# Optimization experiments

Hardware: AMD Instinct MI355X
Metric: run time of the kernel (lower is better)

The kernel has to match this reference:

```python
import jax, jax.numpy as jnp
import numpy as np

REGIONS = [(0, 16), (17, 21), (22, 26), (27, 30), (31, 35), (36, 41), (42, 47), (48, 59), (60, 67)]
LN_EPS = 1e-5


def setup_inputs() -> dict:
    key = jax.random.key(0)
    ks = jax.random.split(key, 8)
    B, T, N, D = 32, 128, 68, 128
    sc = 1.0 / np.sqrt(D)
    inp = {
        "lm_data": jax.random.normal(ks[0], (B, T, N, D), jnp.float32),
        "adj": jax.random.uniform(ks[1], (77, 77), jnp.float32) / 77.0,
        "Wr": jax.random.normal(ks[2], (D, 1), jnp.float32) * sc,
        "br": jnp.zeros((1,), jnp.float32),
        "W0": jax.random.normal(ks[3], (D, D), jnp.float32) * sc,
        "b0": jnp.zeros((D,), jnp.float32),
        "W1": jax.random.normal(ks[4], (D, D), jnp.float32) * sc,
        "b1": jnp.zeros((D,), jnp.float32),
        "W2": jax.random.normal(ks[5], (D, D), jnp.float32) * sc,
        "b2": jnp.zeros((D,), jnp.float32),
        "W3": jax.random.normal(ks[6], (D, D), jnp.float32) * sc,
        "b3": jnp.zeros((D,), jnp.float32),
        "gamma": jnp.ones((D,), jnp.float32),
        "beta": jnp.zeros((D,), jnp.float32),
    }
    return inp


def _region_pool(x, Wr, br):
    # x: [B,T,R,D] -> attention-pooled [B,T,D]
    scores = jnp.einsum('btrd,do->btro', x, Wr) + br  # [B,T,R,1]
    w = jax.nn.softmax(scores, axis=-2)
    return jnp.sum(w * x, axis=-2)


def reference(lm_data, adj, Wr, br, W0, b0, W1, b1, W2, b2, W3, b3, gamma, beta):
    # init_global_nodes: gather each region, attention-pool, scatter into 9 global nodes
    global_nodes = jnp.stack(
        [_region_pool(lm_data[..., s:e + 1, :], Wr, br) for s, e in REGIONS], axis=2
    )  # [B,T,9,D]
    x = jnp.concatenate([lm_data, global_nodes], axis=2)  # [B,T,77,D]

    # 4-layer residual GCN: relu(Linear(adj @ x))
    layers = [(W0, b0), (W1, b1), (W2, b2), (W3, b3)]
    residual = x
    for i, (W, b) in enumerate(layers):
        agg = jnp.einsum('nm,btmd->btnd', adj, x)
        out = jax.nn.relu(agg @ W + b)
        if i < len(layers) - 1:
            out = out + residual  # feature dims all equal
            residual = out
        x = out

    # LayerNorm (dropout is identity at eval)
    mu = jnp.mean(x, axis=-1, keepdims=True)
    var = jnp.var(x, axis=-1, keepdims=True)
    x = (x - mu) / jnp.sqrt(var + LN_EPS) * gamma + beta
    return x
```

## Files before the change

### kernel.cpp

```cpp
#include <hip/hip_runtime.h>
#include <stdint.h>

typedef __attribute__((ext_vector_type(8))) short bf16x8;
typedef __attribute__((ext_vector_type(4))) float f32x4;
typedef unsigned short u16;
typedef __attribute__((ext_vector_type(4))) unsigned short us4;
typedef __attribute__((ext_vector_type(8))) unsigned short us8;

#define NP 80

__device__ __constant__ int c_RS[9] = {0, 17, 22, 27, 31, 36, 42, 48, 60};
__device__ __constant__ int c_RE[9] = {16, 21, 26, 30, 35, 41, 47, 59, 67};

__device__ __forceinline__ float b2f(u16 h) {
    union { unsigned int u; float f; } v;
    v.u = ((unsigned int)h) << 16;
    return v.f;
}
__device__ __forceinline__ u16 f2b(float f) {
    union { float f; unsigned int u; } v;
    v.f = f;
    unsigned int r = v.u + 0x7fffu + ((v.u >> 16) & 1u);
    return (u16)(r >> 16);
}
__device__ __forceinline__ int agx(int row, int col) {
    return row * 128 + (col ^ (((row & 4) << 3) | ((row & 8) << 1)));
}

__global__ void prep_kernel(const float* __restrict__ adj,
                            const float* __restrict__ W0, const float* __restrict__ W1,
                            const float* __restrict__ W2, const float* __restrict__ W3,
                            u16* __restrict__ adjp, u16* __restrict__ WT) {
    int id = blockIdx.x * 256 + threadIdx.x;
    if (id < 80 * 96) {
        int m = id / 96, c = id - m * 96;
        float v = 0.f;
        if (m < 77) {
            int k = (c < 64) ? c : (c - 16);
            if (c >= 64 && c < 80) k = 77;
            if (k < 77) v = adj[m * 77 + k];
        }
        adjp[id] = f2b(v);
    }
    {
        int l = id >> 14, r = id & 16383;
        int n = r >> 7, k = r & 127;
        const float* W = (l == 0) ? W0 : (l == 1) ? W1 : (l == 2) ? W2 : W3;
        WT[id] = f2b(W[k * 128 + n]);
    }
}

__global__ __launch_bounds__(256, 4) void gcn_kernel(
    const float* __restrict__ lm, const float* __restrict__ Wr,
    const float* __restrict__ b0, const float* __restrict__ b1,
    const float* __restrict__ b2, const float* __restrict__ b3,
    const float* __restrict__ gamma, const float* __restrict__ beta,
    const u16* __restrict__ adjp, const u16* __restrict__ WT,
    float* __restrict__ out) {
    __shared__ __align__(16) u16 xT[128 * NP];
    __shared__ __align__(16) u16 ag[80 * 128];

    const int t = threadIdx.x;
    const int lane = t & 63;
    const int w = t >> 6;
    const int lo = lane & 15;
    const int qd = lane >> 4;
    const size_t pos = blockIdx.x;
    const float* lmp = lm + pos * (68 * 128);

    float* WrF = (float*)&ag[68 * 128];
    float* scoreS = (float*)&ag[70 * 128];
    float* muP = (float*)xT;
    float* rsP = muP + 80;

    if (t < 128) {
        WrF[t] = Wr[t];
        xT[t * NP + 77] = 0; xT[t * NP + 78] = 0; xT[t * NP + 79] = 0;
    }
    const float4* lmp4 = (const float4*)lmp;
    for (int c = t; c < 68 * 32; c += 256) {
        int n = c >> 5, q = c & 31;
        float4 v = lmp4[c];
        us4 o;
        o[0] = f2b(v.x); o[1] = f2b(v.y); o[2] = f2b(v.z); o[3] = f2b(v.w);
        *(us4*)(&ag[agx(n, q * 4)]) = o;
    }
    __syncthreads();

    for (int c = t; c < 68 * 16; c += 256) {
        int d8 = c / 68, n = c - d8 * 68;
        us8 v = *(const us8*)(&ag[agx(n, d8 * 8)]);
#pragma unroll
        for (int j = 0; j < 8; j++) xT[(d8 * 8 + j) * NP + n] = v[j];
    }
    if (t < 68) {
        float s = 0.f;
        for (int d8 = 0; d8 < 16; d8++) {
            us8 v = *(const us8*)(&ag[agx(t, d8 * 8)]);
#pragma unroll
            for (int j = 0; j < 8; j++) s += b2f(v[j]) * WrF[d8 * 8 + j];
        }
        scoreS[t] = s;
    }
    __syncthreads();

    for (int c = t; c < 9 * 128; c += 256) {
        int r = c >> 7, d = c & 127;
        int s0 = c_RS[r], e0 = c_RE[r];
        float mx = -3e38f;
        for (int i = s0; i <= e0; i++) mx = fmaxf(mx, scoreS[i]);
        float sum = 0.f, g = 0.f;
        for (int i = s0; i <= e0; i++) {
            float e = __expf(scoreS[i] - mx);
            sum += e;
            g += e * b2f(ag[agx(i, d)]);
        }
        xT[d * NP + 68 + r] = f2b(g / sum);
    }
    __syncthreads();

    for (int l = 0; l < 4; l++) {
        f32x4 acc[5][2];
#pragma unroll
        for (int a = 0; a < 5; a++)
#pragma unroll
            for (int j = 0; j < 2; j++)
#pragma unroll
                for (int r = 0; r < 4; r++) acc[a][j][r] = 0.f;
#pragma unroll
        for (int ks = 0; ks < 3; ks++) {
            const int koff = (ks == 2) ? 48 : ks * 32;
            bf16x8 bA[5], bB[2];
#pragma unroll
            for (int tm = 0; tm < 5; tm++)
                bA[tm] = *(const bf16x8*)(adjp + (tm * 16 + lo) * 96 + ks * 32 + qd * 8);
#pragma unroll
            for (int j = 0; j < 2; j++)
                bB[j] = *(const bf16x8*)(&xT[((w + 4 * j) * 16 + lo) * NP + koff + qd * 8]);
#pragma unroll
            for (int tm = 0; tm < 5; tm++)
#pragma unroll
                for (int j = 0; j < 2; j++)
                    acc[tm][j] = __builtin_amdgcn_mfma_f32_16x16x32_bf16(bA[tm], bB[j], acc[tm][j], 0, 0, 0);
        }
#pragma unroll
        for (int tm = 0; tm < 5; tm++)
#pragma unroll
            for (int j = 0; j < 2; j++) {
                int col = (w + 4 * j) * 16 + lo;
#pragma unroll
                for (int r = 0; r < 4; r++)
                    ag[agx(tm * 16 + qd * 4 + r, col)] = f2b(acc[tm][j][r]);
            }
        __syncthreads();

#pragma unroll
        for (int a = 0; a < 5; a++)
#pragma unroll
            for (int j = 0; j < 2; j++)
#pragma unroll
                for (int r = 0; r < 4; r++) acc[a][j][r] = 0.f;
        const u16* WTl = WT + l * 16384;
#pragma unroll
        for (int ks = 0; ks < 4; ks++) {
            bf16x8 aF[5], bW[2];
#pragma unroll
            for (int tm = 0; tm < 5; tm++)
                aF[tm] = *(const bf16x8*)(&ag[agx(tm * 16 + lo, ks * 32 + qd * 8)]);
#pragma unroll
            for (int j = 0; j < 2; j++)
                bW[j] = *(const bf16x8*)(WTl + ((w + 4 * j) * 16 + lo) * 128 + ks * 32 + qd * 8);
#pragma unroll
            for (int tm = 0; tm < 5; tm++)
#pragma unroll
                for (int j = 0; j < 2; j++)
                    acc[tm][j] = __builtin_amdgcn_mfma_f32_16x16x32_bf16(aF[tm], bW[j], acc[tm][j], 0, 0, 0);
        }
        const float* bl = (l == 0) ? b0 : (l == 1) ? b1 : (l == 2) ? b2 : b3;
        if (l == 3) __syncthreads();
#pragma unroll
        for (int j = 0; j < 2; j++) {
            int col = (w + 4 * j) * 16 + lo;
            float bv = bl[col];
            if (l < 3) {
#pragma unroll
                for (int tm = 0; tm < 5; tm++) {
                    int nb = tm * 16 + qd * 4;
                    us4 old4 = *(const us4*)(&xT[col * NP + nb]);
                    us4 nv;
#pragma unroll
                    for (int r = 0; r < 4; r++) {
                        float v = fmaxf(acc[tm][j][r] + bv, 0.f) + b2f(old4[r]);
                        nv[r] = f2b(v);
                    }
                    *(us4*)(&xT[col * NP + nb]) = nv;
                }
            } else {
#pragma unroll
                for (int tm = 0; tm < 5; tm++)
#pragma unroll
                    for (int r = 0; r < 4; r++)
                        ag[agx(tm * 16 + qd * 4 + r, col)] = f2b(fmaxf(acc[tm][j][r] + bv, 0.f));
            }
        }
        __syncthreads();
    }

    if (t < 154) {
        int n = t >> 1, h = t & 1;
        float s = 0.f, ss = 0.f;
#pragma unroll
        for (int i = 0; i < 8; i++) {
            us8 v = *(const us8*)(&ag[agx(n, h * 64 + i * 8)]);
#pragma unroll
            for (int j = 0; j < 8; j++) { float a = b2f(v[j]); s += a; ss += a * a; }
        }
        s += __shfl_xor(s, 1);
        ss += __shfl_xor(ss, 1);
        if (h == 0) {
            float mu = s * (1.f / 128.f);
            muP[n] = mu;
            rsP[n] = rsqrtf(ss * (1.f / 128.f) - mu * mu + 1e-5f);
        }
    }
    __syncthreads();

    float* outp = out + pos * 9856;
    for (int c = t; c < 77 * 32; c += 256) {
        int n = c >> 5, q = c & 31;
        us4 v = *(const us4*)(&ag[agx(n, q * 4)]);
        float mu = muP[n], rs = rsP[n];
        float4 gm = *(const float4*)(gamma + q * 4);
        float4 bt = *(const float4*)(beta + q * 4);
        float4 o;
        o.x = (b2f(v[0]) - mu) * rs * gm.x + bt.x;
        o.y = (b2f(v[1]) - mu) * rs * gm.y + bt.y;
        o.z = (b2f(v[2]) - mu) * rs * gm.z + bt.z;
        o.w = (b2f(v[3]) - mu) * rs * gm.w + bt.w;
        *(float4*)(outp + n * 128 + q * 4) = o;
    }
}

extern "C" void kernel_launch(void* const* d_in, const int* in_sizes, int n_in,
                              void* d_out, int out_size, void* d_ws, size_t ws_size,
                              hipStream_t stream) {
    const float* lm = (const float*)d_in[0];
    const float* adj = (const float*)d_in[1];
    const float* Wr = (const float*)d_in[2];
    const float* W0 = (const float*)d_in[4];
    const float* b0 = (const float*)d_in[5];
    const float* W1 = (const float*)d_in[6];
    const float* b1 = (const float*)d_in[7];
    const float* W2 = (const float*)d_in[8];
    const float* b2 = (const float*)d_in[9];
    const float* W3 = (const float*)d_in[10];
    const float* b3 = (const float*)d_in[11];
    const float* gamma = (const float*)d_in[12];
    const float* beta = (const float*)d_in[13];

    u16* adjp = (u16*)d_ws;
    u16* WT = (u16*)((char*)d_ws + 80 * 96 * 2);

    prep_kernel<<<256, 256, 0, stream>>>(adj, W0, W1, W2, W3, adjp, WT);
    gcn_kernel<<<4096, 256, 0, stream>>>(lm, Wr, b0, b1, b2, b3, gamma, beta,
                                         adjp, WT, (float*)d_out);
}
```

Measured before the change: 467.6 us.

## Swizzle LDS layouts, use packed bf16 conversions, precompute softmax weights

Changes the XOR swizzle of the row-major activation buffer and adds a swizzle to the transposed buffer, aiming to cut LDS bank conflicts on the MFMA operand loads and the transpose writes. Replaces the manual float-to-bf16 rounding with the HIP library's packed two-element conversion, and uses 32-bit packed bf16 unpacking. Region softmax weights are now computed once per region by 9 threads instead of being recomputed by every pooling thread, and the score dot product is split across two threads per node. This adds one extra barrier and a serial softmax step for those 9 threads.

```diff
diff --git a/kernel.cpp b/kernel.cpp
--- a/kernel.cpp
+++ b/kernel.cpp
@@ -1,10 +1,10 @@
 #include <hip/hip_runtime.h>
+#include <hip/hip_bf16.h>
 #include <stdint.h>
 
 typedef __attribute__((ext_vector_type(8))) short bf16x8;
 typedef __attribute__((ext_vector_type(4))) float f32x4;
 typedef unsigned short u16;
-typedef __attribute__((ext_vector_type(4))) unsigned short us4;
 typedef __attribute__((ext_vector_type(8))) unsigned short us8;
 
 #define NP 80
@@ -12,19 +12,33 @@
 __device__ __constant__ int c_RS[9] = {0, 17, 22, 27, 31, 36, 42, 48, 60};
 __device__ __constant__ int c_RE[9] = {16, 21, 26, 30, 35, 41, 47, 59, 67};
 
+__device__ __forceinline__ u16 f2b(float f) {
+    __hip_bfloat16 h = __float2bfloat16(f);
+    u16 r;
+    __builtin_memcpy(&r, &h, 2);
+    return r;
+}
+__device__ __forceinline__ uint32_t f2b2(float a, float b) {
+    __hip_bfloat162 h = __float22bfloat162_rn(make_float2(a, b));
+    uint32_t r;
+    __builtin_memcpy(&r, &h, 4);
+    return r;
+}
 __device__ __forceinline__ float b2f(u16 h) {
-    union { unsigned int u; float f; } v;
-    v.u = ((unsigned int)h) << 16;
-    return v.f;
-}
-__device__ __forceinline__ u16 f2b(float f) {
-    union { float f; unsigned int u; } v;
-    v.f = f;
-    unsigned int r = v.u + 0x7fffu + ((v.u >> 16) & 1u);
-    return (u16)(r >> 16);
-}
+    union { unsigned int u; float f; } v; v.u = ((unsigned int)h) << 16; return v.f;
+}
+__device__ __forceinline__ float b2f_lo(uint32_t u) {
+    union { unsigned int u; float f; } v; v.u = u << 16; return v.f;
+}
+__device__ __forceinline__ float b2f_hi(uint32_t u) {
+    union { unsigned int u; float f; } v; v.u = u & 0xffff0000u; return v.f;
+}
+
 __device__ __forceinline__ int agx(int row, int col) {
-    return row * 128 + (col ^ (((row & 4) << 3) | ((row & 8) << 1)));
+    return row * 128 + (col ^ ((row & 15) << 3));
+}
+__device__ __forceinline__ int xtx(int f, int n) {
+    return f * NP + (n ^ ((f & 4) << 1));
 }
 
 __global__ void prep_kernel(const float* __restrict__ adj,
@@ -70,20 +84,20 @@
 
     float* WrF = (float*)&ag[68 * 128];
     float* scoreS = (float*)&ag[70 * 128];
+    float* wtS = (float*)&ag[72 * 128];
     float* muP = (float*)xT;
     float* rsP = muP + 80;
 
     if (t < 128) {
         WrF[t] = Wr[t];
-        xT[t * NP + 77] = 0; xT[t * NP + 78] = 0; xT[t * NP + 79] = 0;
+        xT[xtx(t, 77)] = 0; xT[xtx(t, 78)] = 0; xT[xtx(t, 79)] = 0;
     }
     const float4* lmp4 = (const float4*)lmp;
     for (int c = t; c < 68 * 32; c += 256) {
         int n = c >> 5, q = c & 31;
         float4 v = lmp4[c];
-        us4 o;
-        o[0] = f2b(v.x); o[1] = f2b(v.y); o[2] = f2b(v.z); o[3] = f2b(v.w);
-        *(us4*)(&ag[agx(n, q * 4)]) = o;
+        uint2 o = make_uint2(f2b2(v.x, v.y), f2b2(v.z, v.w));
+        *(uint2*)(&ag[agx(n, q * 4)]) = o;
     }
     __syncthreads();
 
@@ -91,31 +105,42 @@
         int d8 = c / 68, n = c - d8 * 68;
         us8 v = *(const us8*)(&ag[agx(n, d8 * 8)]);
 #pragma unroll
-        for (int j = 0; j < 8; j++) xT[(d8 * 8 + j) * NP + n] = v[j];
-    }
-    if (t < 68) {
+        for (int j = 0; j < 8; j++) xT[xtx(d8 * 8 + j, n)] = v[j];
+    }
+    if (t < 136) {
+        int n = t >> 1, h = t & 1;
         float s = 0.f;
-        for (int d8 = 0; d8 < 16; d8++) {
-            us8 v = *(const us8*)(&ag[agx(t, d8 * 8)]);
-#pragma unroll
-            for (int j = 0; j < 8; j++) s += b2f(v[j]) * WrF[d8 * 8 + j];
-        }
-        scoreS[t] = s;
+#pragma unroll
+        for (int i = 0; i < 8; i++) {
+            uint4 v = *(const uint4*)(&ag[agx(n, h * 64 + i * 8)]);
+            const float* wp = WrF + h * 64 + i * 8;
+            s += b2f_lo(v.x) * wp[0] + b2f_hi(v.x) * wp[1]
+               + b2f_lo(v.y) * wp[2] + b2f_hi(v.y) * wp[3]
+               + b2f_lo(v.z) * wp[4] + b2f_hi(v.z) * wp[5]
+               + b2f_lo(v.w) * wp[6] + b2f_hi(v.w) * wp[7];
+        }
+        s += __shfl_xor(s, 1);
+        if (h == 0) scoreS[n] = s;
+    }
+    __syncthreads();
+
+    if (t < 9) {
+        int s0 = c_RS[t], e0 = c_RE[t];
+        float mx = -3e38f;
+        for (int i = s0; i <= e0; i++) mx = fmaxf(mx, scoreS[i]);
+        float sum = 0.f;
+        for (int i = s0; i <= e0; i++) { float e = __expf(scoreS[i] - mx); wtS[i] = e; sum += e; }
+        float inv = 1.f / sum;
+        for (int i = s0; i <= e0; i++) wtS[i] *= inv;
     }
     __syncthreads();
 
     for (int c = t; c < 9 * 128; c += 256) {
         int r = c >> 7, d = c & 127;
         int s0 = c_RS[r], e0 = c_RE[r];
-        float mx = -3e38f;
-        for (int i = s0; i <= e0; i++) mx = fmaxf(mx, scoreS[i]);
-        float sum = 0.f, g = 0.f;
-        for (int i = s0; i <= e0; i++) {
-            float e = __expf(scoreS[i] - mx);
-            sum += e;
-            g += e * b2f(ag[agx(i, d)]);
-        }
-        xT[d * NP + 68 + r] = f2b(g / sum);
+        float g = 0.f;
+        for (int i = s0; i <= e0; i++) g += wtS[i] * b2f(ag[agx(i, d)]);
+        xT[xtx(d, 68 + r)] = f2b(g);
     }
     __syncthreads();
 
@@ -136,7 +161,7 @@
                 bA[tm] = *(const bf16x8*)(adjp + (tm * 16 + lo) * 96 + ks * 32 + qd * 8);
 #pragma unroll
             for (int j = 0; j < 2; j++)
-                bB[j] = *(const bf16x8*)(&xT[((w + 4 * j) * 16 + lo) * NP + koff + qd * 8]);
+                bB[j] = *(const bf16x8*)(&xT[xtx((w + 4 * j) * 16 + lo, koff + qd * 8)]);
 #pragma unroll
             for (int tm = 0; tm < 5; tm++)
 #pragma unroll
@@ -186,14 +211,13 @@
 #pragma unroll
                 for (int tm = 0; tm < 5; tm++) {
                     int nb = tm * 16 + qd * 4;
-                    us4 old4 = *(const us4*)(&xT[col * NP + nb]);
-                    us4 nv;
-#pragma unroll
-                    for (int r = 0; r < 4; r++) {
-                        float v = fmaxf(acc[tm][j][r] + bv, 0.f) + b2f(old4[r]);
-                        nv[r] = f2b(v);
-                    }
-                    *(us4*)(&xT[col * NP + nb]) = nv;
+                    uint2 old4 = *(const uint2*)(&xT[xtx(col, nb)]);
+                    float v0 = fmaxf(acc[tm][j][0] + bv, 0.f) + b2f_lo(old4.x);
+                    float v1 = fmaxf(acc[tm][j][1] + bv, 0.f) + b2f_hi(old4.x);
+                    float v2 = fmaxf(acc[tm][j][2] + bv, 0.f) + b2f_lo(old4.y);
+                    float v3 = fmaxf(acc[tm][j][3] + bv, 0.f) + b2f_hi(old4.y);
+                    uint2 nv = make_uint2(f2b2(v0, v1), f2b2(v2, v3));
+                    *(uint2*)(&xT[xtx(col, nb)]) = nv;
                 }
             } else {
 #pragma unroll
@@ -211,9 +235,16 @@
         float s = 0.f, ss = 0.f;
 #pragma unroll
         for (int i = 0; i < 8; i++) {
-            us8 v = *(const us8*)(&ag[agx(n, h * 64 + i * 8)]);
-#pragma unroll
-            for (int j = 0; j < 8; j++) { float a = b2f(v[j]); s += a; ss += a * a; }
+            uint4 v = *(const uint4*)(&ag[agx(n, h * 64 + i * 8)]);
+            float a;
+            a = b2f_lo(v.x); s += a; ss += a * a;
+            a = b2f_hi(v.x); s += a; ss += a * a;
+            a = b2f_lo(v.y); s += a; ss += a * a;
+            a = b2f_hi(v.y); s += a; ss += a * a;
+            a = b2f_lo(v.z); s += a; ss += a * a;
+            a = b2f_hi(v.z); s += a; ss += a * a;
+            a = b2f_lo(v.w); s += a; ss += a * a;
+            a = b2f_hi(v.w); s += a; ss += a * a;
         }
         s += __shfl_xor(s, 1);
         ss += __shfl_xor(ss, 1);
@@ -228,15 +259,15 @@
     float* outp = out + pos * 9856;
     for (int c = t; c < 77 * 32; c += 256) {
         int n = c >> 5, q = c & 31;
-        us4 v = *(const us4*)(&ag[agx(n, q * 4)]);
+        uint2 v = *(const uint2*)(&ag[agx(n, q * 4)]);
         float mu = muP[n], rs = rsP[n];
         float4 gm = *(const float4*)(gamma + q * 4);
         float4 bt = *(const float4*)(beta + q * 4);
         float4 o;
-        o.x = (b2f(v[0]) - mu) * rs * gm.x + bt.x;
-        o.y = (b2f(v[1]) - mu) * rs * gm.y + bt.y;
-        o.z = (b2f(v[2]) - mu) * rs * gm.z + bt.z;
-        o.w = (b2f(v[3]) - mu) * rs * gm.w + bt.w;
+        o.x = (b2f_lo(v.x) - mu) * rs * gm.x + bt.x;
+        o.y = (b2f_hi(v.x) - mu) * rs * gm.y + bt.y;
+        o.z = (b2f_lo(v.y) - mu) * rs * gm.z + bt.z;
+        o.w = (b2f_hi(v.y) - mu) * rs * gm.w + bt.w;
         *(float4*)(outp + n * 128 + q * 4) = o;
     }
 }
```

Result: slower. 692.5 us (+48.1%).
